# Kernel optimization log

Hardware: AMD Instinct MI355X
Metric: run time of the kernel (lower is better)

## Reference

```python
import jax, jax.numpy as jnp
import numpy as np

HIDDEN = 4096
N_HEADS = 32
HEAD_DIM = HIDDEN // N_HEADS  # 128, rotary_dim == head_dim
ROPE_BASE = 10000.0


def apply_rope(x, positions):
    # x: [B, S, n_heads, head_dim]; positions: [B, S] int. GPT-NeoX style (half split).
    hd = x.shape[-1]
    inv_freq = 1.0 / (ROPE_BASE ** (jnp.arange(0, hd, 2, dtype=jnp.float32) / hd))
    freqs = positions.astype(jnp.float32)[..., None] * inv_freq  # [B, S, hd/2]
    cos = jnp.cos(freqs)[:, :, None, :]  # [B, S, 1, hd/2]
    sin = jnp.sin(freqs)[:, :, None, :]
    x1, x2 = jnp.split(x, 2, axis=-1)
    return jnp.concatenate([x1 * cos - x2 * sin, x2 * cos + x1 * sin], axis=-1)


def setup_inputs() -> dict:
    key = jax.random.key(0)
    k1, k2, k3 = jax.random.split(key, 3)
    B, S = 2, 2048
    hidden_states = jax.random.normal(k1, (B, S, HIDDEN), dtype=jnp.float32)
    positions = jnp.broadcast_to(jnp.arange(S, dtype=jnp.int32), (B, S))
    # nn.Linear(hidden, 3*hidden, bias=False): weight [3*hidden, hidden]
    W_pack = jax.random.normal(k2, (3 * HIDDEN, HIDDEN), dtype=jnp.float32) * (HIDDEN ** -0.5)
    W_o = jax.random.normal(k3, (HIDDEN, HIDDEN), dtype=jnp.float32) * (HIDDEN ** -0.5)
    return {"hidden_states": hidden_states, "positions": positions, "W_pack": W_pack, "W_o": W_o}


def reference(hidden_states, positions, W_pack, W_o):
    B, S, H = hidden_states.shape
    scale = HEAD_DIM ** -0.5
    proj = hidden_states @ W_pack.T            # [B, S, 3H]
    q, k, v = jnp.split(proj, 3, axis=-1)
    q = q.reshape(B, S, N_HEADS, HEAD_DIM)
    k = k.reshape(B, S, N_HEADS, HEAD_DIM)
    v = v.reshape(B, S, N_HEADS, HEAD_DIM)
    q = apply_rope(q, positions)
    k = apply_rope(k, positions)
    scores = jnp.einsum("bqnd,bknd->bnqk", q, k) * scale  # [B, n, S, S]
    causal = jnp.tril(jnp.ones((S, S), dtype=bool))
    scores = jnp.where(causal, scores, jnp.finfo(scores.dtype).min)
    probs = jax.nn.softmax(scores, axis=-1)
    attn = jnp.einsum("bnqk,bknd->bqnd", probs, v).reshape(B, S, H)
    return attn @ W_o.T
```

## Files before the change

kernel.cpp:

```cpp
#include <hip/hip_runtime.h>
#include <stdint.h>

#define HIDDEN 4096
#define NHEADS 32
#define HD 128
#define SEQ 2048
#define NTOK 4096
#define QKVN 12288

typedef __attribute__((ext_vector_type(8))) short frag8;
typedef __attribute__((ext_vector_type(4))) float fl4;

__device__ __forceinline__ unsigned short f2b(float f) {
    unsigned u = __float_as_uint(f);
    return (unsigned short)((u + 0x7FFFu + ((u >> 16) & 1u)) >> 16);
}
__device__ __forceinline__ float b2f(unsigned short h) {
    return __uint_as_float(((unsigned)h) << 16);
}
__device__ __forceinline__ void gl_lds16(const void* g, void* l) {
    __builtin_amdgcn_global_load_lds(
        (const __attribute__((address_space(1))) unsigned int*)(uintptr_t)g,
        (__attribute__((address_space(3))) unsigned int*)(uintptr_t)l,
        16, 0, 0);
}

__global__ void cvt_f32_bf16(const float* __restrict__ src,
                             unsigned short* __restrict__ dst, int n8) {
    int i = blockIdx.x * 256 + threadIdx.x;
    if (i >= n8) return;
    long e = (long)i * 8;
    fl4 a = *(const fl4*)(src + e);
    fl4 b = *(const fl4*)(src + e + 4);
    union { unsigned short us[8]; frag8 v; } o;
    o.us[0] = f2b(a[0]); o.us[1] = f2b(a[1]); o.us[2] = f2b(a[2]); o.us[3] = f2b(a[3]);
    o.us[4] = f2b(b[0]); o.us[5] = f2b(b[1]); o.us[6] = f2b(b[2]); o.us[7] = f2b(b[3]);
    *(frag8*)(dst + e) = o.v;
}

__global__ void rope_kernel(unsigned short* __restrict__ proj,
                            const int* __restrict__ positions) {
    int tid = blockIdx.x * 256 + threadIdx.x;
    int j  = tid & 63;
    int h  = (tid >> 6) & 31;
    int qk = (tid >> 11) & 1;
    int t  = tid >> 12;
    int pos = positions[t];
    float inv = powf(10000.0f, -(float)j * (1.0f / 64.0f));
    float fr = (float)pos * inv;
    float sv, cv;
    sincosf(fr, &sv, &cv);
    unsigned short* base = proj + (long)t * QKVN + qk * HIDDEN + h * HD;
    float x1 = b2f(base[j]);
    float x2 = b2f(base[j + 64]);
    base[j]      = f2b(x1 * cv - x2 * sv);
    base[j + 64] = f2b(x2 * cv + x1 * sv);
}

template <int OUT_F32>
__global__ __launch_bounds__(512, 2) void gemm256(
    const unsigned short* __restrict__ A,
    const unsigned short* __restrict__ B,
    void* __restrict__ Cv, int M, int N, int K) {
    __shared__ unsigned short lds[65536];
    const int tid = threadIdx.x, lane = tid & 63, w = tid >> 6;
    const int wr = w >> 2, wc = w & 3;
    const int fr = lane & 15, quad = lane >> 4;

    const int gx = gridDim.x;
    const int nwg = gx * gridDim.y;
    int bid = blockIdx.y * gx + blockIdx.x;
    const int cpx = nwg >> 3;
    int swz = (bid & 7) * cpx + (bid >> 3);
    const long n0 = (long)(swz % gx) * 256;
    const long m0 = (long)(swz / gx) * 256;

    const int r0 = w * 8 + (lane >> 3);
    const int scol = ((lane ^ (lane >> 3)) & 7) * 8;
    const int dofs = w * 512 + lane * 8;
    const unsigned short* Ag = A + (m0 + r0) * (long)K + scol;
    const unsigned short* Bg = B + (n0 + r0) * (long)K + scol;
    auto stg = [&](unsigned short* Lh, const unsigned short* G, long t) {
        gl_lds16(G + t * 64, Lh + dofs);
        gl_lds16(G + t * 64 + (long)K * 64, Lh + dofs + 4096);
    };
#define STGA(s, h, t) stg(lds + (s)*32768 + (h)*8192, Ag + (long)(h) * 128 * K, (t))
#define STGB(s, h, t) stg(lds + (s)*32768 + 16384 + (h)*8192, Bg + (long)(h) * 128 * K, (t))

    const int qx8 = (quad ^ (fr & 3)) * 8;
    const int kx0 = (fr >> 2) & 1;
    const int arow = wr * 64 + fr;
    const int brow = wc * 32 + fr;

    frag8 af[4][2], bf0[2][2], bf1[2][2];
    fl4 acc[2][2][4][2];
    fl4 z = {0.f, 0.f, 0.f, 0.f};
#pragma unroll
    for (int qm = 0; qm < 2; ++qm)
#pragma unroll
        for (int qn = 0; qn < 2; ++qn)
#pragma unroll
            for (int mi = 0; mi < 4; ++mi)
#pragma unroll
                for (int ni = 0; ni < 2; ++ni) acc[qm][qn][mi][ni] = z;

#define LDA(h)                                                                   \
    _Pragma("unroll") for (int mi = 0; mi < 4; ++mi) {                           \
        af[mi][0] = *(const frag8*)(Lc + (h)*8192 + (arow + mi * 16) * 64 +      \
                                    (kx0 << 5) + qx8);                           \
        af[mi][1] = *(const frag8*)(Lc + (h)*8192 + (arow + mi * 16) * 64 +      \
                                    ((1 ^ kx0) << 5) + qx8);                     \
    }
#define LDB(h, BF)                                                               \
    _Pragma("unroll") for (int ni = 0; ni < 2; ++ni) {                           \
        BF[ni][0] = *(const frag8*)(Lc + 16384 + (h)*8192 +                      \
                                    (brow + ni * 16) * 64 + (kx0 << 5) + qx8);   \
        BF[ni][1] = *(const frag8*)(Lc + 16384 + (h)*8192 +                      \
                                    (brow + ni * 16) * 64 + ((1 ^ kx0) << 5) +   \
                                    qx8);                                        \
    }
#define MF(qm, qn, BF)                                                           \
    __builtin_amdgcn_s_setprio(1);                                               \
    _Pragma("unroll") for (int mi = 0; mi < 4; ++mi)                             \
        _Pragma("unroll") for (int ni = 0; ni < 2; ++ni) {                       \
        acc[qm][qn][mi][ni] = __builtin_amdgcn_mfma_f32_16x16x32_bf16(           \
            af[mi][0], BF[ni][0], acc[qm][qn][mi][ni], 0, 0, 0);                 \
        acc[qm][qn][mi][ni] = __builtin_amdgcn_mfma_f32_16x16x32_bf16(           \
            af[mi][1], BF[ni][1], acc[qm][qn][mi][ni], 0, 0, 0);                 \
    }                                                                            \
    __builtin_amdgcn_s_setprio(0);

#define KTILE(s, T)                                                              \
    {                                                                            \
        unsigned short* Lc = lds + (s)*32768;                                    \
        const long t1 = ((T) + 1 < nt) ? (T) + 1 : nt - 1;                       \
        const long t2 = ((T) + 2 < nt) ? (T) + 2 : nt - 1;                       \
        LDA(0);                                                                  \
        LDB(0, bf0);                                                             \
        STGA((s) ^ 1, 1, t1);                                                    \
        __builtin_amdgcn_s_barrier();                                            \
        asm volatile("s_waitcnt lgkmcnt(0)" ::: "memory");                       \
        MF(0, 0, bf0);                                                           \
        __builtin_amdgcn_s_barrier();                                            \
        LDB(1, bf1);                                                             \
        STGA((s), 0, t2);                                                        \
        __builtin_amdgcn_s_barrier();                                            \
        asm volatile("s_waitcnt lgkmcnt(0)" ::: "memory");                       \
        MF(0, 1, bf1);                                                           \
        __builtin_amdgcn_s_barrier();                                            \
        LDA(1);                                                                  \
        STGB((s), 0, t2);                                                        \
        __builtin_amdgcn_s_barrier();                                            \
        asm volatile("s_waitcnt lgkmcnt(0)" ::: "memory");                       \
        MF(1, 0, bf0);                                                           \
        __builtin_amdgcn_s_barrier();                                            \
        STGB((s), 1, t2);                                                        \
        asm volatile("s_waitcnt vmcnt(6)" ::: "memory");                         \
        __builtin_amdgcn_s_barrier();                                            \
        MF(1, 1, bf1);                                                           \
        __builtin_amdgcn_s_barrier();                                            \
    }

    const int nt = K >> 6;
    STGA(0, 0, 0);
    STGB(0, 0, 0);
    STGB(0, 1, 0);
    STGA(0, 1, 0);
    STGA(1, 0, 1);
    STGB(1, 0, 1);
    STGB(1, 1, 1);
    asm volatile("s_waitcnt vmcnt(6)" ::: "memory");
    __builtin_amdgcn_s_barrier();

    for (int T = 0; T < nt; T += 2) {
        KTILE(0, T);
        KTILE(1, T + 1);
    }
    asm volatile("s_waitcnt vmcnt(0)" ::: "memory");

#pragma unroll
    for (int qm = 0; qm < 2; ++qm)
#pragma unroll
        for (int qn = 0; qn < 2; ++qn)
#pragma unroll
            for (int mi = 0; mi < 4; ++mi)
#pragma unroll
                for (int ni = 0; ni < 2; ++ni)
#pragma unroll
                    for (int r = 0; r < 4; ++r) {
                        long row = m0 + qm * 128 + wr * 64 + mi * 16 + quad * 4 + r;
                        long col = n0 + qn * 128 + wc * 32 + ni * 16 + fr;
                        float v = acc[qm][qn][mi][ni][r];
                        if (OUT_F32)
                            ((float*)Cv)[row * N + col] = v;
                        else
                            ((unsigned short*)Cv)[row * N + col] = f2b(v);
                    }
#undef STGA
#undef STGB
#undef LDA
#undef LDB
#undef MF
#undef KTILE
}

__global__ __launch_bounds__(256, 2) void attn_kernel(
    const unsigned short* __restrict__ proj,
    unsigned short* __restrict__ out) {
    __shared__ unsigned short Ks[64 * 128];
    __shared__ unsigned short Vt[128 * 80];
    __shared__ unsigned short Ps[4][32 * 88];

    const int qt = (int)gridDim.x - 1 - (int)blockIdx.x;
    const int h = blockIdx.y;
    const int b = blockIdx.z;
    const int tid = threadIdx.x, lane = tid & 63, w = tid >> 6;
    const int q0 = qt * 128;
    const int fr = lane & 15, quad = lane >> 4;
    const int fq = quad * 8;
    const long tokbase = (long)b * SEQ;
    const float scale = 0.08838834764831845f;
    fl4 z = {0.f, 0.f, 0.f, 0.f};

    frag8 qf[2][4];
#pragma unroll
    for (int mi = 0; mi < 2; mi++)
#pragma unroll
        for (int kc = 0; kc < 4; kc++) {
            int qrow = q0 + w * 32 + mi * 16 + fr;
            qf[mi][kc] = *(const frag8*)(proj + (tokbase + qrow) * QKVN +
                                         h * HD + kc * 32 + fq);
        }

    fl4 o[2][8];
#pragma unroll
    for (int mi = 0; mi < 2; mi++)
#pragma unroll
        for (int n = 0; n < 8; n++) o[mi][n] = z;
    float m_i[2][4], l_i[2][4];
#pragma unroll
    for (int mi = 0; mi < 2; mi++)
#pragma unroll
        for (int r = 0; r < 4; r++) { m_i[mi][r] = -1e30f; l_i[mi][r] = 0.f; }

    const int ksrow = w * 4 + (lane >> 4);
    const int kphys = (lane & 15) * 8;
    const int kgcol = ((lane & 15) ^ ksrow) * 8;
    const int vrow = lane;
    const int vdc = w * 32;

    const int ktiles = (q0 + 128) / 64;
    for (int kt = 0; kt < ktiles; kt++) {
        const int k0 = kt * 64;
        __syncthreads();
#pragma unroll
        for (int c = 0; c < 4; c++) {
            long tok = tokbase + k0 + c * 16 + ksrow;
            gl_lds16(proj + tok * QKVN + HIDDEN + h * HD + kgcol,
                     Ks + (c * 16 + ksrow) * 128 + kphys);
        }
        {
            const unsigned short* vp =
                proj + (tokbase + k0 + vrow) * QKVN + 2 * HIDDEN + h * HD + vdc;
#pragma unroll
            for (int u = 0; u < 4; u++) {
                frag8 vv = *(const frag8*)(vp + u * 8);
#pragma unroll
                for (int e = 0; e < 8; e++)
                    Vt[(vdc + u * 8 + e) * 80 + vrow] = (unsigned short)vv[e];
            }
        }
        __syncthreads();

        fl4 sc[2][4];
#pragma unroll
        for (int kn = 0; kn < 4; kn++) {
            frag8 kf[4];
#pragma unroll
            for (int kc = 0; kc < 4; kc++)
                kf[kc] = *(const frag8*)(Ks + (kn * 16 + fr) * 128 +
                                         ((kc * 4 + quad) ^ fr) * 8);
#pragma unroll
            for (int mi = 0; mi < 2; mi++) {
                fl4 a = z;
#pragma unroll
                for (int kc = 0; kc < 4; kc++)
                    a = __builtin_amdgcn_mfma_f32_16x16x32_bf16(qf[mi][kc],
                                                                kf[kc], a, 0, 0, 0);
                sc[mi][kn] = a;
            }
        }
#pragma unroll
        for (int mi = 0; mi < 2; mi++) {
#pragma unroll
            for (int r = 0; r < 4; r++) {
                int qrow = q0 + w * 32 + mi * 16 + quad * 4 + r;
                float sv4[4];
                float mx = -1e30f;
#pragma unroll
                for (int kn = 0; kn < 4; kn++) {
                    int kcol = k0 + kn * 16 + fr;
                    float s = sc[mi][kn][r] * scale;
                    s = (kcol <= qrow) ? s : -1e30f;
                    sv4[kn] = s;
                    mx = fmaxf(mx, s);
                }
#pragma unroll
                for (int off = 1; off < 16; off <<= 1)
                    mx = fmaxf(mx, __shfl_xor(mx, off, 64));
                float mold = m_i[mi][r];
                float mnew = fmaxf(mold, mx);
                float alpha = __expf(mold - mnew);
                float rsum = 0.f;
#pragma unroll
                for (int kn = 0; kn < 4; kn++) {
                    float p = __expf(sv4[kn] - mnew);
                    unsigned short pb = f2b(p);
                    Ps[w][(mi * 16 + quad * 4 + r) * 88 + kn * 16 + fr] = pb;
                    rsum += b2f(pb);
                }
#pragma unroll
                for (int off = 1; off < 16; off <<= 1)
                    rsum += __shfl_xor(rsum, off, 64);
                l_i[mi][r] = l_i[mi][r] * alpha + rsum;
                m_i[mi][r] = mnew;
#pragma unroll
                for (int n = 0; n < 8; n++) o[mi][n][r] *= alpha;
            }
        }
        frag8 pf[2][2];
#pragma unroll
        for (int mi = 0; mi < 2; mi++)
#pragma unroll
            for (int kc = 0; kc < 2; kc++)
                pf[mi][kc] =
                    *(const frag8*)(Ps[w] + (mi * 16 + fr) * 88 + kc * 32 + fq);
#pragma unroll
        for (int n = 0; n < 8; n++) {
            frag8 vf0 = *(const frag8*)(Vt + (n * 16 + fr) * 80 + fq);
            frag8 vf1 = *(const frag8*)(Vt + (n * 16 + fr) * 80 + 32 + fq);
#pragma unroll
            for (int mi = 0; mi < 2; mi++) {
                o[mi][n] = __builtin_amdgcn_mfma_f32_16x16x32_bf16(pf[mi][0], vf0,
                                                                   o[mi][n], 0, 0, 0);
                o[mi][n] = __builtin_amdgcn_mfma_f32_16x16x32_bf16(pf[mi][1], vf1,
                                                                   o[mi][n], 0, 0, 0);
            }
        }
    }
#pragma unroll
    for (int mi = 0; mi < 2; mi++)
#pragma unroll
        for (int n = 0; n < 8; n++)
#pragma unroll
            for (int r = 0; r < 4; r++) {
                int qrow = q0 + w * 32 + mi * 16 + quad * 4 + r;
                float val = o[mi][n][r] / l_i[mi][r];
                out[(tokbase + qrow) * HIDDEN + h * HD + n * 16 + fr] = f2b(val);
            }
}

extern "C" void kernel_launch(void* const* d_in, const int* in_sizes, int n_in,
                              void* d_out, int out_size, void* d_ws, size_t ws_size,
                              hipStream_t stream) {
    const float* hs = (const float*)d_in[0];
    const int* pos  = (const int*)d_in[1];
    const float* wp = (const float*)d_in[2];
    const float* wo = (const float*)d_in[3];
    float* out = (float*)d_out;

    char* ws = (char*)d_ws;
    unsigned short* Xb    = (unsigned short*)ws;
    unsigned short* Wpb   = (unsigned short*)(ws + 33554432L);
    unsigned short* proj  = (unsigned short*)(ws + 134217728L);
    unsigned short* attnb = Wpb;
    unsigned short* Wob   = Xb;

    cvt_f32_bf16<<<(16777216 / 8) / 256, 256, 0, stream>>>(hs, Xb, 16777216 / 8);
    cvt_f32_bf16<<<(50331648 / 8) / 256, 256, 0, stream>>>(wp, Wpb, 50331648 / 8);
    gemm256<0><<<dim3(QKVN / 256, NTOK / 256), 512, 0, stream>>>(
        Xb, Wpb, (void*)proj, NTOK, QKVN, HIDDEN);
    rope_kernel<<<16777216 / 256, 256, 0, stream>>>(proj, pos);
    attn_kernel<<<dim3(SEQ / 128, NHEADS, 2), 256, 0, stream>>>(proj, attnb);
    cvt_f32_bf16<<<(16777216 / 8) / 256, 256, 0, stream>>>(wo, Wob, 16777216 / 8);
    gemm256<1><<<dim3(HIDDEN / 256, NTOK / 256), 512, 0, stream>>>(
        attnb, Wob, d_out, NTOK, HIDDEN, HIDDEN);
}
```

Measured before the change: 1.201 ms.

## Transpose score MFMA and use lazy softmax rescaling in flash attention

The QK^T MFMA operands are swapped so each lane holds one query row's scores. Row max and sum then need only two cross-lane shuffles instead of four per row. The running max is rescaled lazily, only when some wave's max grows by more than 8, and P is written to LDS as packed 64-bit stores. RoPE switches to fast exp2 and the __sinf/__cosf intrinsics, which can lose accuracy for large position angles.

Result: faster. 1.091 ms (-9.1%).

```diff
diff --git a/kernel.cpp b/kernel.cpp
--- a/kernel.cpp
+++ b/kernel.cpp
@@ -46,10 +46,9 @@
     int qk = (tid >> 11) & 1;
     int t  = tid >> 12;
     int pos = positions[t];
-    float inv = powf(10000.0f, -(float)j * (1.0f / 64.0f));
+    float inv = __builtin_amdgcn_exp2f(-0.20762051f * (float)j);
     float fr = (float)pos * inv;
-    float sv, cv;
-    sincosf(fr, &sv, &cv);
+    float sv = __sinf(fr), cv = __cosf(fr);
     unsigned short* base = proj + (long)t * QKVN + qk * HIDDEN + h * HD;
     float x1 = b2f(base[j]);
     float x2 = b2f(base[j + 64]);
@@ -237,11 +236,9 @@
     for (int mi = 0; mi < 2; mi++)
 #pragma unroll
         for (int n = 0; n < 8; n++) o[mi][n] = z;
-    float m_i[2][4], l_i[2][4];
-#pragma unroll
-    for (int mi = 0; mi < 2; mi++)
-#pragma unroll
-        for (int r = 0; r < 4; r++) { m_i[mi][r] = -1e30f; l_i[mi][r] = 0.f; }
+    float m_i[2], l_i[2];
+    m_i[0] = m_i[1] = -1e30f;
+    l_i[0] = l_i[1] = 0.f;
 
     const int ksrow = w * 4 + (lane >> 4);
     const int kphys = (lane & 15) * 8;
@@ -285,49 +282,72 @@
                 fl4 a = z;
 #pragma unroll
                 for (int kc = 0; kc < 4; kc++)
-                    a = __builtin_amdgcn_mfma_f32_16x16x32_bf16(qf[mi][kc],
-                                                                kf[kc], a, 0, 0, 0);
+                    a = __builtin_amdgcn_mfma_f32_16x16x32_bf16(kf[kc],
+                                                                qf[mi][kc], a, 0, 0, 0);
                 sc[mi][kn] = a;
             }
         }
+
+        float mx2[2];
 #pragma unroll
         for (int mi = 0; mi < 2; mi++) {
-#pragma unroll
-            for (int r = 0; r < 4; r++) {
-                int qrow = q0 + w * 32 + mi * 16 + quad * 4 + r;
-                float sv4[4];
-                float mx = -1e30f;
-#pragma unroll
-                for (int kn = 0; kn < 4; kn++) {
-                    int kcol = k0 + kn * 16 + fr;
+            const int qrow = q0 + w * 32 + mi * 16 + fr;
+            float mxv = -1e30f;
+#pragma unroll
+            for (int kn = 0; kn < 4; kn++) {
+                const int kbase = k0 + kn * 16 + quad * 4;
+#pragma unroll
+                for (int r = 0; r < 4; r++) {
                     float s = sc[mi][kn][r] * scale;
-                    s = (kcol <= qrow) ? s : -1e30f;
-                    sv4[kn] = s;
-                    mx = fmaxf(mx, s);
+                    s = (kbase + r <= qrow) ? s : -1e30f;
+                    sc[mi][kn][r] = s;
+                    mxv = fmaxf(mxv, s);
                 }
-#pragma unroll
-                for (int off = 1; off < 16; off <<= 1)
-                    mx = fmaxf(mx, __shfl_xor(mx, off, 64));
-                float mold = m_i[mi][r];
-                float mnew = fmaxf(mold, mx);
-                float alpha = __expf(mold - mnew);
-                float rsum = 0.f;
-#pragma unroll
-                for (int kn = 0; kn < 4; kn++) {
-                    float p = __expf(sv4[kn] - mnew);
-                    unsigned short pb = f2b(p);
-                    Ps[w][(mi * 16 + quad * 4 + r) * 88 + kn * 16 + fr] = pb;
-                    rsum += b2f(pb);
+            }
+            mxv = fmaxf(mxv, __shfl_xor(mxv, 16, 64));
+            mxv = fmaxf(mxv, __shfl_xor(mxv, 32, 64));
+            mx2[mi] = mxv;
+        }
+        bool need = (mx2[0] > m_i[0] + 8.0f) || (mx2[1] > m_i[1] + 8.0f);
+        if (__any(need)) {
+            float alpha[2];
+#pragma unroll
+            for (int mi = 0; mi < 2; mi++) {
+                float mnew = fmaxf(m_i[mi], mx2[mi]);
+                alpha[mi] = __expf(m_i[mi] - mnew);
+                m_i[mi] = mnew;
+                l_i[mi] *= alpha[mi];
+            }
+#pragma unroll
+            for (int mi = 0; mi < 2; mi++)
+#pragma unroll
+                for (int rr = 0; rr < 4; rr++) {
+                    float af = __shfl(alpha[mi], (lane & 48) | (quad * 4 + rr), 64);
+#pragma unroll
+                    for (int n = 0; n < 8; n++) o[mi][n][rr] *= af;
                 }
-#pragma unroll
-                for (int off = 1; off < 16; off <<= 1)
-                    rsum += __shfl_xor(rsum, off, 64);
-                l_i[mi][r] = l_i[mi][r] * alpha + rsum;
-                m_i[mi][r] = mnew;
-#pragma unroll
-                for (int n = 0; n < 8; n++) o[mi][n][r] *= alpha;
-            }
-        }
+        }
+#pragma unroll
+        for (int mi = 0; mi < 2; mi++) {
+            float rsum = 0.f;
+            const float m = m_i[mi];
+#pragma unroll
+            for (int kn = 0; kn < 4; kn++) {
+                union { unsigned short us[4]; unsigned long long u; } pk;
+#pragma unroll
+                for (int r = 0; r < 4; r++) {
+                    float p = __expf(sc[mi][kn][r] - m);
+                    pk.us[r] = f2b(p);
+                    rsum += b2f(pk.us[r]);
+                }
+                *(unsigned long long*)(&Ps[w][(mi * 16 + fr) * 88 + kn * 16 +
+                                              quad * 4]) = pk.u;
+            }
+            rsum += __shfl_xor(rsum, 16, 64);
+            rsum += __shfl_xor(rsum, 32, 64);
+            l_i[mi] += rsum;
+        }
+
         frag8 pf[2][2];
 #pragma unroll
         for (int mi = 0; mi < 2; mi++)
@@ -351,13 +371,15 @@
 #pragma unroll
     for (int mi = 0; mi < 2; mi++)
 #pragma unroll
-        for (int n = 0; n < 8; n++)
-#pragma unroll
-            for (int r = 0; r < 4; r++) {
-                int qrow = q0 + w * 32 + mi * 16 + quad * 4 + r;
-                float val = o[mi][n][r] / l_i[mi][r];
-                out[(tokbase + qrow) * HIDDEN + h * HD + n * 16 + fr] = f2b(val);
-            }
+        for (int rr = 0; rr < 4; rr++) {
+            float lf = __shfl(l_i[mi], (lane & 48) | (quad * 4 + rr), 64);
+            float rl = 1.0f / lf;
+            int qrow = q0 + w * 32 + mi * 16 + quad * 4 + rr;
+#pragma unroll
+            for (int n = 0; n < 8; n++)
+                out[(tokbase + qrow) * HIDDEN + h * HD + n * 16 + fr] =
+                    f2b(o[mi][n][rr] * rl);
+        }
 }
 
 extern "C" void kernel_launch(void* const* d_in, const int* in_sizes, int n_in,
```
